# Kernel optimization log

Measured on AMD Instinct MI355X. Metric: run time of the kernel, lower is better.

Reference implementation:

```python
import jax, jax.numpy as jnp
import numpy as np

S, B, D, H = 2048, 2, 1024, 16
DK = D // H
E, F = 8, 4096


def layernorm(x, g, b, eps=1e-5):
    mu = x.mean(-1, keepdims=True)
    var = x.var(-1, keepdims=True)
    return (x - mu) / jnp.sqrt(var + eps) * g + b


def setup_inputs() -> dict:
    key = jax.random.key(0)
    ks = jax.random.split(key, 10)
    s = 0.02
    rn = lambda k, shape: jax.random.normal(k, shape, jnp.float32) * s
    return dict(
        x=jax.random.normal(ks[0], (S, B, D), jnp.float32),
        ln1_g=jnp.ones((D,), jnp.float32), ln1_b=jnp.zeros((D,), jnp.float32),
        ln2_g=jnp.ones((D,), jnp.float32), ln2_b=jnp.zeros((D,), jnp.float32),
        wq=rn(ks[1], (D, D)), bq=jnp.zeros((D,), jnp.float32),
        wk=rn(ks[2], (D, D)), bk=jnp.zeros((D,), jnp.float32),
        wv=rn(ks[3], (D, D)), bv=jnp.zeros((D,), jnp.float32),
        wo=rn(ks[4], (D, D)), bo=jnp.zeros((D,), jnp.float32),
        w_gate=rn(ks[5], (D, E)), b_gate=jnp.zeros((E,), jnp.float32),
        w1=rn(ks[6], (E, D, F)), b1=jnp.zeros((E, F), jnp.float32),
        w2=rn(ks[7], (E, F, D)), b2=jnp.zeros((E, D), jnp.float32),
        mask=jnp.ones((S, S, B), jnp.bool_),
    )


def reference(x, ln1_g, ln1_b, ln2_g, ln2_b, wq, bq, wk, bk, wv, bv, wo, bo,
              w_gate, b_gate, w1, b1, w2, b2, mask):
    scale = 1.0 / np.sqrt(DK).astype(np.float32)
    # --- self attention (pre-norm) ---
    z = layernorm(x, ln1_g, ln1_b)
    q = (z @ wq + bq).reshape(S, B, H, DK)
    k = (z @ wk + bk).reshape(S, B, H, DK)
    v = (z @ wv + bv).reshape(S, B, H, DK)
    scores = jnp.einsum('sbhd,tbhd->stbh', q, k) * scale  # [Sq,Sk,B,H]
    scores = jnp.where(mask[:, :, :, None], scores, -jnp.inf)
    attn = jax.nn.softmax(scores, axis=1)  # softmax over key axis (dim=1)
    o = jnp.einsum('stbh,tbhd->sbhd', attn, v).reshape(S, B, D)
    x = x + (o @ wo + bo)
    # --- switch (top-1) MoE FFN (pre-norm) ---
    z = layernorm(x, ln2_g, ln2_b)
    flat = z.reshape(-1, D)  # [T, D], T = S*B
    probs = jax.nn.softmax(flat @ w_gate + b_gate, axis=-1)  # [T, E]
    pmax = probs.max(-1)
    routes = probs.argmax(-1)
    onehot = jax.nn.one_hot(routes, E, dtype=flat.dtype)  # [T, E]
    # dense dispatch: compute every expert, combine with one-hot mask
    h = jax.nn.relu(jnp.einsum('td,edf->etf', flat, w1) + b1[:, None, :])
    y = jnp.einsum('etf,efd->etd', h, w2) + b2[:, None, :]
    ff = jnp.einsum('etd,te->td', y, onehot) * pmax[:, None]
    out = x + ff.reshape(S, B, D)
    counts = onehot.sum(0)  # tokens per expert
    route_prob_sum = probs.sum(0)
    n_dropped = jnp.array(0, jnp.int32)  # drop_tokens=False
    return out, counts, route_prob_sum, n_dropped, pmax
```

## Files before the change

kernel.cpp:

```cpp
#include <hip/hip_runtime.h>

#define S_LEN 2048
#define B_SZ 2
#define D_DIM 1024
#define H_HEADS 16
#define DK_DIM 64
#define E_EXP 8
#define F_DIM 4096
#define T_TOK 4096

typedef unsigned short ush;
typedef __bf16 bf16x8 __attribute__((ext_vector_type(8)));
typedef float f32x4 __attribute__((ext_vector_type(4)));

__device__ __forceinline__ ush f2bf(float f) {
  union { __bf16 h; ush u; } cv;
  cv.h = (__bf16)f;
  return cv.u;
}

__device__ __forceinline__ float bf2f(ush u) {
  union { unsigned int i; float f; } cv;
  cv.i = ((unsigned int)u) << 16;
  return cv.f;
}

__device__ __forceinline__ void split2(float v, ush& h, ush& l) {
  ush hh = f2bf(v);
  h = hh;
  l = f2bf(v - bf2f(hh));
}

__device__ __forceinline__ void gload16(const void* g, void* l) {
  __builtin_amdgcn_global_load_lds(
      (const __attribute__((address_space(1))) unsigned int*)g,
      (__attribute__((address_space(3))) unsigned int*)l, 16, 0, 0);
}

#define MFMA(a, b, c) __builtin_amdgcn_mfma_f32_16x16x32_bf16(a, b, c, 0, 0, 0)

__global__ __launch_bounds__(256) void ln1_split(const float* __restrict__ x,
    const float* __restrict__ g, const float* __restrict__ b,
    ush* __restrict__ zh, ush* __restrict__ zl) {
  int t = blockIdx.x;
  float4 v = ((const float4*)(x + (size_t)t * D_DIM))[threadIdx.x];
  float s = v.x + v.y + v.z + v.w;
  float s2 = v.x * v.x + v.y * v.y + v.z * v.z + v.w * v.w;
#pragma unroll
  for (int off = 32; off > 0; off >>= 1) {
    s += __shfl_down(s, off);
    s2 += __shfl_down(s2, off);
  }
  __shared__ float red[8];
  int wid = threadIdx.x >> 6;
  if ((threadIdx.x & 63) == 0) { red[wid] = s; red[4 + wid] = s2; }
  __syncthreads();
  float sum = red[0] + red[1] + red[2] + red[3];
  float sq = red[4] + red[5] + red[6] + red[7];
  float mu = sum * (1.0f / D_DIM);
  float var = sq * (1.0f / D_DIM) - mu * mu;
  float rstd = rsqrtf(var + 1e-5f);
  float4 gg = ((const float4*)g)[threadIdx.x];
  float4 bb = ((const float4*)b)[threadIdx.x];
  float o[4];
  o[0] = (v.x - mu) * rstd * gg.x + bb.x;
  o[1] = (v.y - mu) * rstd * gg.y + bb.y;
  o[2] = (v.z - mu) * rstd * gg.z + bb.z;
  o[3] = (v.w - mu) * rstd * gg.w + bb.w;
  ushort4 uh, ul;
  split2(o[0], uh.x, ul.x); split2(o[1], uh.y, ul.y);
  split2(o[2], uh.z, ul.z); split2(o[3], uh.w, ul.w);
  *(ushort4*)(zh + (size_t)t * D_DIM + threadIdx.x * 4) = uh;
  *(ushort4*)(zl + (size_t)t * D_DIM + threadIdx.x * 4) = ul;
}

__global__ __launch_bounds__(256) void transpose_split(const float* __restrict__ in,
    ush* __restrict__ outh, ush* __restrict__ outl, int R, int C) {
  __shared__ float tile[32][33];
  int c0 = blockIdx.x * 32, r0 = blockIdx.y * 32;
  int tx = threadIdx.x & 31, ty = threadIdx.x >> 5;
#pragma unroll
  for (int i = 0; i < 4; i++)
    tile[ty + i * 8][tx] = in[(size_t)(r0 + ty + i * 8) * C + c0 + tx];
  __syncthreads();
#pragma unroll
  for (int i = 0; i < 4; i++) {
    float v = tile[tx][ty + i * 8];
    ush h, l;
    split2(v, h, l);
    size_t idx = (size_t)(c0 + ty + i * 8) * R + r0 + tx;
    outh[idx] = h;
    outl[idx] = l;
  }
}

__global__ __launch_bounds__(256) void transpose_bf16(const float* __restrict__ in,
    ush* __restrict__ out, int R, int C) {
  __shared__ float tile[32][33];
  int e = blockIdx.z;
  const float* ip = in + (size_t)e * R * C;
  ush* op = out + (size_t)e * R * C;
  int c0 = blockIdx.x * 32, r0 = blockIdx.y * 32;
  int tx = threadIdx.x & 31, ty = threadIdx.x >> 5;
#pragma unroll
  for (int i = 0; i < 4; i++)
    tile[ty + i * 8][tx] = ip[(size_t)(r0 + ty + i * 8) * C + c0 + tx];
  __syncthreads();
#pragma unroll
  for (int i = 0; i < 4; i++)
    op[(size_t)(c0 + ty + i * 8) * R + r0 + tx] = f2bf(tile[tx][ty + i * 8]);
}

__device__ __forceinline__ void split_gemm(const ush* __restrict__ Ah,
    const ush* __restrict__ Al, int lda, const ush* __restrict__ Bh,
    const ush* __restrict__ Bl, int ldb, int K, int tid, f32x4 acc[4][4],
    ush (*Ash)[64], ush (*Asl)[64], ush (*Bsh)[64], ush (*Bsl)[64]) {
  int lane = tid & 63, w = tid >> 6, quad = lane >> 4, ln15 = lane & 15;
  int srow = tid >> 3, scol = (tid & 7) * 8;
  int mb = (w >> 1) * 64, nb = (w & 1) * 64;
  for (int kb = 0; kb < K; kb += 64) {
    __syncthreads();
#pragma unroll
    for (int r = 0; r < 4; r++) {
      int rr = r * 32 + srow;
      gload16(Ah + (size_t)rr * lda + kb + scol, &Ash[rr][scol]);
      gload16(Al + (size_t)rr * lda + kb + scol, &Asl[rr][scol]);
      gload16(Bh + (size_t)rr * ldb + kb + scol, &Bsh[rr][scol]);
      gload16(Bl + (size_t)rr * ldb + kb + scol, &Bsl[rr][scol]);
    }
    __syncthreads();
#pragma unroll
    for (int kc = 0; kc < 2; kc++) {
      int kof = kc * 32 + quad * 8;
      bf16x8 avh[4], avl[4], bvh[4], bvl[4];
#pragma unroll
      for (int i = 0; i < 4; i++) {
        avh[i] = *(const bf16x8*)&Ash[mb + i * 16 + ln15][kof];
        avl[i] = *(const bf16x8*)&Asl[mb + i * 16 + ln15][kof];
        bvh[i] = *(const bf16x8*)&Bsh[nb + i * 16 + ln15][kof];
        bvl[i] = *(const bf16x8*)&Bsl[nb + i * 16 + ln15][kof];
      }
#pragma unroll
      for (int mi = 0; mi < 4; mi++)
#pragma unroll
        for (int ni = 0; ni < 4; ni++) {
          acc[mi][ni] = MFMA(avh[mi], bvh[ni], acc[mi][ni]);
          acc[mi][ni] = MFMA(avh[mi], bvl[ni], acc[mi][ni]);
          acc[mi][ni] = MFMA(avl[mi], bvh[ni], acc[mi][ni]);
        }
    }
  }
}

__global__ __launch_bounds__(256) void qkv_mfma(const ush* __restrict__ zh,
    const ush* __restrict__ zl, const ush* __restrict__ wT,
    const float* __restrict__ bq, const float* __restrict__ bk,
    const float* __restrict__ bv, ush* __restrict__ qh_, ush* __restrict__ kh_,
    ush* __restrict__ vth_) {
  __shared__ ush Ash[128][64], Asl[128][64], Bsh[128][64], Bsl[128][64];
  int z = blockIdx.z;
  int m0 = blockIdx.x * 128, n0 = blockIdx.y * 128;
  const ush* Bh = wT + (size_t)z * 2097152;
  const ush* Bl = Bh + 1048576;
  const float* bias = (z == 0) ? bq : (z == 1) ? bk : bv;
  ush* outh = (z == 0) ? qh_ : (z == 1) ? kh_ : vth_;
  int tid = threadIdx.x, lane = tid & 63, w = tid >> 6;
  int quad = lane >> 4, ln15 = lane & 15;
  int mb = (w >> 1) * 64, nb = (w & 1) * 64;
  f32x4 acc[4][4] = {};
  split_gemm(zh + (size_t)m0 * D_DIM, zl + (size_t)m0 * D_DIM, D_DIM,
             Bh + (size_t)n0 * D_DIM, Bl + (size_t)n0 * D_DIM, D_DIM, D_DIM,
             tid, acc, Ash, Asl, Bsh, Bsl);
#pragma unroll
  for (int mi = 0; mi < 4; mi++)
#pragma unroll
    for (int reg = 0; reg < 4; reg++) {
      int m = m0 + mb + mi * 16 + quad * 4 + reg;
      int s = m >> 1, b = m & 1;
#pragma unroll
      for (int ni = 0; ni < 4; ni++) {
        int n = n0 + nb + ni * 16 + ln15;
        float val = acc[mi][ni][reg] + bias[n];
        ush hh, ll;
        split2(val, hh, ll);
        int h = n >> 6, dk = n & 63;
        size_t idx;
        if (z < 2) idx = ((size_t)(b * H_HEADS + h) * S_LEN + s) * DK_DIM + dk;
        else       idx = ((size_t)(b * H_HEADS + h) * DK_DIM + dk) * S_LEN + s;
        outh[idx] = hh;
        outh[idx + 4194304] = ll;
      }
    }
}

__global__ __launch_bounds__(256, 2) void attn_mfma(const ush* __restrict__ qh,
    const ush* __restrict__ ql, const ush* __restrict__ kh,
    const ush* __restrict__ kl, const ush* __restrict__ vth,
    const ush* __restrict__ vtl, ush* __restrict__ oh, ush* __restrict__ ol) {
  int bh = blockIdx.y, q0 = blockIdx.x * 128;
  const size_t hoff = (size_t)bh * S_LEN * DK_DIM;
  __shared__ ush smem[32768];
  ush* Qh_ = smem;
  ush* Ql_ = smem + 8192;
  ush* Kh_ = smem + 16384;
  ush* Kl_ = smem + 20480;
  ush* Vh_ = smem + 24576;
  ush* Vl_ = smem + 28672;
  int tid = threadIdx.x, lane = tid & 63, w = tid >> 6;
  int quad = lane >> 4, ln15 = lane & 15;
  int srow = tid >> 3;
  int schunk = tid & 7;
  int gch = ((schunk ^ (srow & 7))) * 8;
  int sw = ln15 & 7;
#pragma unroll
  for (int p = 0; p < 4; p++) {
    int r = p * 32 + srow;
    gload16(qh + hoff + (size_t)(q0 + r) * DK_DIM + gch, Qh_ + r * 64 + schunk * 8);
    gload16(ql + hoff + (size_t)(q0 + r) * DK_DIM + gch, Ql_ + r * 64 + schunk * 8);
  }
  __syncthreads();
  bf16x8 Qf[2][2][2];
#pragma unroll
  for (int mi = 0; mi < 2; mi++)
#pragma unroll
    for (int kc = 0; kc < 2; kc++) {
      int row = w * 32 + mi * 16 + ln15;
      int ch = ((kc * 4 + quad) ^ sw) * 8;
      Qf[mi][kc][0] = *(const bf16x8*)(Qh_ + row * 64 + ch);
      Qf[mi][kc][1] = *(const bf16x8*)(Ql_ + row * 64 + ch);
    }
  f32x4 Oacc[2][4] = {};
  float m_i[2][4], l_i[2][4];
#pragma unroll
  for (int mi = 0; mi < 2; mi++)
#pragma unroll
    for (int r = 0; r < 4; r++) { m_i[mi][r] = -1e30f; l_i[mi][r] = 0.f; }
  for (int kt = 0; kt < S_LEN / 64; kt++) {
    __syncthreads();
#pragma unroll
    for (int p = 0; p < 2; p++) {
      int r = p * 32 + srow;
      gload16(kh + hoff + (size_t)(kt * 64 + r) * DK_DIM + gch, Kh_ + r * 64 + schunk * 8);
      gload16(kl + hoff + (size_t)(kt * 64 + r) * DK_DIM + gch, Kl_ + r * 64 + schunk * 8);
      gload16(vth + hoff + (size_t)r * S_LEN + kt * 64 + gch, Vh_ + r * 64 + schunk * 8);
      gload16(vtl + hoff + (size_t)r * S_LEN + kt * 64 + gch, Vl_ + r * 64 + schunk * 8);
    }
    __syncthreads();
    f32x4 S[2][4] = {};
#pragma unroll
    for (int kc = 0; kc < 2; kc++) {
      int ch = ((kc * 4 + quad) ^ sw) * 8;
      bf16x8 bkh[4], bkl[4];
#pragma unroll
      for (int ni = 0; ni < 4; ni++) {
        int row = ni * 16 + ln15;
        bkh[ni] = *(const bf16x8*)(Kh_ + row * 64 + ch);
        bkl[ni] = *(const bf16x8*)(Kl_ + row * 64 + ch);
      }
#pragma unroll
      for (int mi = 0; mi < 2; mi++)
#pragma unroll
        for (int ni = 0; ni < 4; ni++) {
          S[mi][ni] = MFMA(Qf[mi][kc][0], bkh[ni], S[mi][ni]);
          S[mi][ni] = MFMA(Qf[mi][kc][0], bkl[ni], S[mi][ni]);
          S[mi][ni] = MFMA(Qf[mi][kc][1], bkh[ni], S[mi][ni]);
        }
    }
#pragma unroll
    for (int mi = 0; mi < 2; mi++)
#pragma unroll
      for (int ni = 0; ni < 4; ni++)
#pragma unroll
        for (int reg = 0; reg < 4; reg++) S[mi][ni][reg] *= 0.125f;
    float mt[2][4];
#pragma unroll
    for (int mi = 0; mi < 2; mi++)
#pragma unroll
      for (int reg = 0; reg < 4; reg++)
        mt[mi][reg] = fmaxf(fmaxf(S[mi][0][reg], S[mi][1][reg]),
                            fmaxf(S[mi][2][reg], S[mi][3][reg]));
#pragma unroll
    for (int x = 1; x < 16; x <<= 1)
#pragma unroll
      for (int mi = 0; mi < 2; mi++)
#pragma unroll
        for (int reg = 0; reg < 4; reg++)
          mt[mi][reg] = fmaxf(mt[mi][reg], __shfl_xor(mt[mi][reg], x));
    float alpha[2][4];
#pragma unroll
    for (int mi = 0; mi < 2; mi++)
#pragma unroll
      for (int reg = 0; reg < 4; reg++) {
        float mnew = fmaxf(m_i[mi][reg], mt[mi][reg]);
        alpha[mi][reg] = expf(m_i[mi][reg] - mnew);
        m_i[mi][reg] = mnew;
      }
    float ls[2][4] = {};
#pragma unroll
    for (int mi = 0; mi < 2; mi++)
#pragma unroll
      for (int ni = 0; ni < 4; ni++)
#pragma unroll
        for (int reg = 0; reg < 4; reg++) {
          float p = expf(S[mi][ni][reg] - m_i[mi][reg]);
          ls[mi][reg] += p;
          ush hh, ll;
          split2(p, hh, ll);
          int row = w * 32 + mi * 16 + quad * 4 + reg;
          int cph = ((ni * 2 + (ln15 >> 3)) ^ ((quad * 4 + reg) & 7)) * 8 + (ln15 & 7);
          Qh_[row * 64 + cph] = hh;
          Ql_[row * 64 + cph] = ll;
        }
#pragma unroll
    for (int x = 1; x < 16; x <<= 1)
#pragma unroll
      for (int mi = 0; mi < 2; mi++)
#pragma unroll
        for (int reg = 0; reg < 4; reg++)
          ls[mi][reg] += __shfl_xor(ls[mi][reg], x);
#pragma unroll
    for (int mi = 0; mi < 2; mi++)
#pragma unroll
      for (int reg = 0; reg < 4; reg++)
        l_i[mi][reg] = l_i[mi][reg] * alpha[mi][reg] + ls[mi][reg];
#pragma unroll
    for (int mi = 0; mi < 2; mi++)
#pragma unroll
      for (int ni = 0; ni < 4; ni++)
#pragma unroll
        for (int reg = 0; reg < 4; reg++) Oacc[mi][ni][reg] *= alpha[mi][reg];
#pragma unroll
    for (int kc = 0; kc < 2; kc++) {
      int ch = ((kc * 4 + quad) ^ sw) * 8;
      bf16x8 aph[2], apl[2], bvh[4], bvl[4];
#pragma unroll
      for (int mi = 0; mi < 2; mi++) {
        int row = w * 32 + mi * 16 + ln15;
        aph[mi] = *(const bf16x8*)(Qh_ + row * 64 + ch);
        apl[mi] = *(const bf16x8*)(Ql_ + row * 64 + ch);
      }
#pragma unroll
      for (int ni = 0; ni < 4; ni++) {
        int row = ni * 16 + ln15;
        bvh[ni] = *(const bf16x8*)(Vh_ + row * 64 + ch);
        bvl[ni] = *(const bf16x8*)(Vl_ + row * 64 + ch);
      }
#pragma unroll
      for (int mi = 0; mi < 2; mi++)
#pragma unroll
        for (int ni = 0; ni < 4; ni++) {
          Oacc[mi][ni] = MFMA(aph[mi], bvh[ni], Oacc[mi][ni]);
          Oacc[mi][ni] = MFMA(aph[mi], bvl[ni], Oacc[mi][ni]);
          Oacc[mi][ni] = MFMA(apl[mi], bvh[ni], Oacc[mi][ni]);
        }
    }
  }
  float inv[2][4];
#pragma unroll
  for (int mi = 0; mi < 2; mi++)
#pragma unroll
    for (int reg = 0; reg < 4; reg++) inv[mi][reg] = 1.0f / l_i[mi][reg];
  int b = bh >> 4, h = bh & 15;
#pragma unroll
  for (int mi = 0; mi < 2; mi++)
#pragma unroll
    for (int ni = 0; ni < 4; ni++)
#pragma unroll
      for (int reg = 0; reg < 4; reg++) {
        float ov = Oacc[mi][ni][reg] * inv[mi][reg];
        int s = q0 + w * 32 + mi * 16 + quad * 4 + reg;
        int col = h * DK_DIM + ni * 16 + ln15;
        size_t idx = (size_t)(s * B_SZ + b) * D_DIM + col;
        ush hh, ll;
        split2(ov, hh, ll);
        oh[idx] = hh;
        ol[idx] = ll;
      }
}

__global__ __launch_bounds__(256) void wo_mfma(const ush* __restrict__ oh,
    const ush* __restrict__ ol, const ush* __restrict__ woTh,
    const float* __restrict__ bo, const float* __restrict__ x,
    float* __restrict__ out) {
  __shared__ ush Ash[128][64], Asl[128][64], Bsh[128][64], Bsl[128][64];
  int m0 = blockIdx.x * 128, n0 = blockIdx.y * 128;
  const ush* Bl = woTh + 1048576;
  int tid = threadIdx.x, lane = tid & 63, w = tid >> 6;
  int quad = lane >> 4, ln15 = lane & 15;
  int mb = (w >> 1) * 64, nb = (w & 1) * 64;
  f32x4 acc[4][4] = {};
  split_gemm(oh + (size_t)m0 * D_DIM, ol + (size_t)m0 * D_DIM, D_DIM,
             woTh + (size_t)n0 * D_DIM, Bl + (size_t)n0 * D_DIM, D_DIM, D_DIM,
             tid, acc, Ash, Asl, Bsh, Bsl);
#pragma unroll
  for (int mi = 0; mi < 4; mi++)
#pragma unroll
    for (int reg = 0; reg < 4; reg++) {
      int m = m0 + mb + mi * 16 + quad * 4 + reg;
#pragma unroll
      for (int ni = 0; ni < 4; ni++) {
        int n = n0 + nb + ni * 16 + ln15;
        size_t idx = (size_t)m * D_DIM + n;
        out[idx] = x[idx] + acc[mi][ni][reg] + bo[n];
      }
    }
}

__global__ __launch_bounds__(256) void moe1_mfma(const ush* __restrict__ zb,
    const ush* __restrict__ w1t, const float* __restrict__ b1,
    const int* __restrict__ list, const int* __restrict__ offs,
    ush* __restrict__ h) {
  int e = blockIdx.x;
  int n0 = blockIdx.y * 128;
  int mhalf = blockIdx.z;
  int off = offs[e], cnt = offs[e + 1] - off;
  __shared__ ush As[128][64], Bs[128][64];
  int tid = threadIdx.x, lane = tid & 63, w = tid >> 6;
  int colb = (lane & 7) * 8;
  int srw = w * 8 + (lane >> 3);
  const ush* gB[4];
  ush* lB[4];
#pragma unroll
  for (int r = 0; r < 4; r++) {
    int row = r * 32 + srw;
    gB[r] = w1t + ((size_t)e * F_DIM + n0 + row) * D_DIM + colb;
    lB[r] = &Bs[row][colb];
  }
  int mb = (w >> 1) * 64, nb = (w & 1) * 64;
  int quad = lane >> 4, ln15 = lane & 15;
  const float* be = b1 + (size_t)e * F_DIM;
  for (int m0 = mhalf * 128; m0 < cnt; m0 += 256) {
    const ush* gA[4];
    ush* lA[4];
#pragma unroll
    for (int r = 0; r < 4; r++) {
      int row = r * 32 + srw;
      int ra = m0 + row; if (ra > cnt - 1) ra = cnt - 1;
      int tok = list[off + ra];
      gA[r] = zb + (size_t)tok * D_DIM + colb;
      lA[r] = &As[row][colb];
    }
    f32x4 acc[4][4] = {};
    for (int kb = 0; kb < D_DIM; kb += 64) {
      __syncthreads();
#pragma unroll
      for (int r = 0; r < 4; r++) { gload16(gA[r] + kb, lA[r]); gload16(gB[r] + kb, lB[r]); }
      __syncthreads();
#pragma unroll
      for (int kc = 0; kc < 2; kc++) {
        int kof = kc * 32 + quad * 8;
        bf16x8 av[4], bv[4];
#pragma unroll
        for (int i = 0; i < 4; i++) {
          av[i] = *(const bf16x8*)&As[mb + i * 16 + ln15][kof];
          bv[i] = *(const bf16x8*)&Bs[nb + i * 16 + ln15][kof];
        }
#pragma unroll
        for (int mi = 0; mi < 4; mi++)
#pragma unroll
          for (int ni = 0; ni < 4; ni++)
            acc[mi][ni] = MFMA(av[mi], bv[ni], acc[mi][ni]);
      }
    }
#pragma unroll
    for (int mi = 0; mi < 4; mi++)
#pragma unroll
      for (int reg = 0; reg < 4; reg++) {
        int lm = m0 + mb + mi * 16 + quad * 4 + reg;
        if (lm < cnt) {
#pragma unroll
          for (int ni = 0; ni < 4; ni++) {
            int n = n0 + nb + ni * 16 + ln15;
            float v = acc[mi][ni][reg] + be[n];
            h[(size_t)(off + lm) * F_DIM + n] = f2bf(fmaxf(v, 0.f));
          }
        }
      }
  }
}

__global__ __launch_bounds__(256) void moe2_mfma(const ush* __restrict__ hb,
    const ush* __restrict__ w2t, const float* __restrict__ b2,
    const int* __restrict__ list, const int* __restrict__ offs,
    const float* __restrict__ pmax, float* __restrict__ out) {
  int e = blockIdx.x;
  int n0 = blockIdx.y * 128;
  int ks = blockIdx.z >> 1;
  int mhalf = blockIdx.z & 1;
  int off = offs[e], cnt = offs[e + 1] - off;
  size_t kbase = (size_t)ks * 1024;
  __shared__ ush As[128][64], Bs[128][64];
  int tid = threadIdx.x, lane = tid & 63, w = tid >> 6;
  int colb = (lane & 7) * 8;
  int srw = w * 8 + (lane >> 3);
  const ush* gB[4];
  ush* lB[4];
#pragma unroll
  for (int r = 0; r < 4; r++) {
    int row = r * 32 + srw;
    gB[r] = w2t + ((size_t)e * D_DIM + n0 + row) * F_DIM + kbase + colb;
    lB[r] = &Bs[row][colb];
  }
  int mb = (w >> 1) * 64, nb = (w & 1) * 64;
  int quad = lane >> 4, ln15 = lane & 15;
  const float* be = b2 + (size_t)e * D_DIM;
  for (int m0 = mhalf * 128; m0 < cnt; m0 += 256) {
    const ush* gA[4];
    ush* lA[4];
#pragma unroll
    for (int r = 0; r < 4; r++) {
      int row = r * 32 + srw;
      int ra = m0 + row; if (ra > cnt - 1) ra = cnt - 1;
      gA[r] = hb + (size_t)(off + ra) * F_DIM + kbase + colb;
      lA[r] = &As[row][colb];
    }
    f32x4 acc[4][4] = {};
    for (int kb = 0; kb < 1024; kb += 64) {
      __syncthreads();
#pragma unroll
      for (int r = 0; r < 4; r++) { gload16(gA[r] + kb, lA[r]); gload16(gB[r] + kb, lB[r]); }
      __syncthreads();
#pragma unroll
      for (int kc = 0; kc < 2; kc++) {
        int kof = kc * 32 + quad * 8;
        bf16x8 av[4], bv[4];
#pragma unroll
        for (int i = 0; i < 4; i++) {
          av[i] = *(const bf16x8*)&As[mb + i * 16 + ln15][kof];
          bv[i] = *(const bf16x8*)&Bs[nb + i * 16 + ln15][kof];
        }
#pragma unroll
        for (int mi = 0; mi < 4; mi++)
#pragma unroll
          for (int ni = 0; ni < 4; ni++)
            acc[mi][ni] = MFMA(av[mi], bv[ni], acc[mi][ni]);
      }
    }
#pragma unroll
    for (int mi = 0; mi < 4; mi++)
#pragma unroll
      for (int reg = 0; reg < 4; reg++) {
        int lm = m0 + mb + mi * 16 + quad * 4 + reg;
        if (lm < cnt) {
          int tok = list[off + lm];
          float p = pmax[tok];
#pragma unroll
          for (int ni = 0; ni < 4; ni++) {
            int n = n0 + nb + ni * 16 + ln15;
            float v = acc[mi][ni][reg];
            if (ks == 0) v += be[n];
            atomicAdd(&out[(size_t)tok * D_DIM + n], v * p);
          }
        }
      }
  }
}

__global__ __launch_bounds__(256) void ln2_gate(const float* __restrict__ x,
    const float* __restrict__ g, const float* __restrict__ b,
    const float* __restrict__ wg, const float* __restrict__ bg,
    ush* __restrict__ zb, float* __restrict__ pmax_out, int* __restrict__ route,
    float* __restrict__ rps_partial) {
  int t = blockIdx.x;
  float4 v = ((const float4*)(x + (size_t)t * D_DIM))[threadIdx.x];
  float s = v.x + v.y + v.z + v.w;
  float s2 = v.x * v.x + v.y * v.y + v.z * v.z + v.w * v.w;
#pragma unroll
  for (int off = 32; off > 0; off >>= 1) {
    s += __shfl_down(s, off);
    s2 += __shfl_down(s2, off);
  }
  __shared__ float red[8];
  int wid = threadIdx.x >> 6;
  if ((threadIdx.x & 63) == 0) { red[wid] = s; red[4 + wid] = s2; }
  __syncthreads();
  float sum = red[0] + red[1] + red[2] + red[3];
  float sq = red[4] + red[5] + red[6] + red[7];
  float mu = sum * (1.0f / D_DIM);
  float var = sq * (1.0f / D_DIM) - mu * mu;
  float rstd = rsqrtf(var + 1e-5f);
  float4 gg = ((const float4*)g)[threadIdx.x];
  float4 bb = ((const float4*)b)[threadIdx.x];
  float zz[4];
  zz[0] = (v.x - mu) * rstd * gg.x + bb.x;
  zz[1] = (v.y - mu) * rstd * gg.y + bb.y;
  zz[2] = (v.z - mu) * rstd * gg.z + bb.z;
  zz[3] = (v.w - mu) * rstd * gg.w + bb.w;
  ushort4 u;
  u.x = f2bf(zz[0]); u.y = f2bf(zz[1]); u.z = f2bf(zz[2]); u.w = f2bf(zz[3]);
  *(ushort4*)(zb + (size_t)t * D_DIM + threadIdx.x * 4) = u;
  int d0 = threadIdx.x * 4;
  float acc[8] = {};
  const float* w0 = wg + (size_t)d0 * E_EXP;
#pragma unroll
  for (int i = 0; i < 4; i++)
#pragma unroll
    for (int e = 0; e < 8; e++)
      acc[e] += zz[i] * w0[i * 8 + e];
#pragma unroll
  for (int off = 32; off > 0; off >>= 1)
#pragma unroll
    for (int e = 0; e < 8; e++) acc[e] += __shfl_down(acc[e], off);
  __shared__ float red2[4][8];
  if ((threadIdx.x & 63) == 0)
#pragma unroll
    for (int e = 0; e < 8; e++) red2[threadIdx.x >> 6][e] = acc[e];
  __syncthreads();
  if (threadIdx.x == 0) {
    float lg[8];
#pragma unroll
    for (int e = 0; e < 8; e++)
      lg[e] = red2[0][e] + red2[1][e] + red2[2][e] + red2[3][e] + bg[e];
    float mx = lg[0];
    int am = 0;
#pragma unroll
    for (int e = 1; e < 8; e++)
      if (lg[e] > mx) { mx = lg[e]; am = e; }
    float se = 0.f, pe[8];
#pragma unroll
    for (int e = 0; e < 8; e++) { pe[e] = expf(lg[e] - mx); se += pe[e]; }
    float inv = 1.0f / se;
    pmax_out[t] = inv;
    route[t] = am;
#pragma unroll
    for (int e = 0; e < 8; e++) rps_partial[(size_t)t * 8 + e] = pe[e] * inv;
  }
}

__global__ __launch_bounds__(256) void reduce_gate(const float* __restrict__ rps_partial,
    const int* __restrict__ route, float* __restrict__ rps, int* __restrict__ counts) {
  int e = blockIdx.x;
  float s = 0.f;
  int c = 0;
  for (int t = threadIdx.x; t < T_TOK; t += 256) {
    s += rps_partial[(size_t)t * 8 + e];
    c += (route[t] == e) ? 1 : 0;
  }
#pragma unroll
  for (int off = 32; off > 0; off >>= 1) {
    s += __shfl_down(s, off);
    c += __shfl_down(c, off);
  }
  __shared__ float sred[4];
  __shared__ int cred[4];
  int wid = threadIdx.x >> 6;
  if ((threadIdx.x & 63) == 0) { sred[wid] = s; cred[wid] = c; }
  __syncthreads();
  if (threadIdx.x == 0) {
    rps[e] = sred[0] + sred[1] + sred[2] + sred[3];
    counts[e] = cred[0] + cred[1] + cred[2] + cred[3];
  }
}

__global__ void init_kernel(int* cursor) {
  int i = threadIdx.x;
  if (i < E_EXP) cursor[i] = 0;
}

__global__ void offsets_kernel(const int* counts, int* offs, float* counts_f, float* ndrop) {
  if (threadIdx.x == 0) {
    int o = 0;
    for (int e = 0; e < E_EXP; e++) { offs[e] = o; o += counts[e]; }
    offs[E_EXP] = o;
    for (int e = 0; e < E_EXP; e++) counts_f[e] = (float)counts[e];
    *ndrop = 0.f;
  }
}

__global__ void scatter_kernel(const int* __restrict__ route, const int* __restrict__ offs,
                               int* __restrict__ cursor, int* __restrict__ list) {
  int t = blockIdx.x * 256 + threadIdx.x;
  int lane = threadIdx.x & 63;
  int e = (t < T_TOK) ? route[t] : -1;
#pragma unroll
  for (int ex = 0; ex < E_EXP; ex++) {
    unsigned long long mask = __ballot(e == ex);
    int cntw = __popcll(mask);
    if (cntw) {
      int leader = __ffsll((unsigned long long)mask) - 1;
      int base = 0;
      if (lane == leader) base = atomicAdd(&cursor[ex], cntw);
      base = __shfl(base, leader);
      if (e == ex) {
        int rank = __popcll(mask & ((1ull << lane) - 1));
        list[offs[ex] + base + rank] = t;
      }
    }
  }
}

extern "C" void kernel_launch(void* const* d_in, const int* in_sizes, int n_in,
                              void* d_out, int out_size, void* d_ws, size_t ws_size,
                              hipStream_t stream) {
  const float* x = (const float*)d_in[0];
  const float* ln1_g = (const float*)d_in[1];
  const float* ln1_b = (const float*)d_in[2];
  const float* ln2_g = (const float*)d_in[3];
  const float* ln2_b = (const float*)d_in[4];
  const float* wq = (const float*)d_in[5];
  const float* bq = (const float*)d_in[6];
  const float* wk = (const float*)d_in[7];
  const float* bk = (const float*)d_in[8];
  const float* wv = (const float*)d_in[9];
  const float* bv = (const float*)d_in[10];
  const float* wo = (const float*)d_in[11];
  const float* bo = (const float*)d_in[12];
  const float* wg = (const float*)d_in[13];
  const float* bg = (const float*)d_in[14];
  const float* w1 = (const float*)d_in[15];
  const float* b1 = (const float*)d_in[16];
  const float* w2 = (const float*)d_in[17];
  const float* b2 = (const float*)d_in[18];

  float* out = (float*)d_out;
  float* counts_f = out + (size_t)T_TOK * D_DIM;
  float* rps = counts_f + E_EXP;
  float* ndrop = rps + E_EXP;
  float* pmax = ndrop + 1;

  const size_t MB1 = 1048576;
  char* base = (char*)d_ws;
  ush* zh  = (ush*)(base + 0 * MB1);
  ush* zl  = (ush*)(base + 8 * MB1);
  ush* qh  = (ush*)(base + 16 * MB1);
  ush* ql  = (ush*)(base + 24 * MB1);
  ush* kh  = (ush*)(base + 32 * MB1);
  ush* kl  = (ush*)(base + 40 * MB1);
  ush* vth = (ush*)(base + 48 * MB1);
  ush* vtl = (ush*)(base + 56 * MB1);
  ush* wT  = (ush*)(base + 64 * MB1);
  ush* oh  = (ush*)(base + 80 * MB1);
  ush* ol  = (ush*)(base + 88 * MB1);
  ush* zb  = (ush*)(base + 64 * MB1);
  ush* hb  = (ush*)(base + 72 * MB1);
  int* route  = (int*)(base + 104 * MB1);
  int* list   = route + T_TOK;
  int* counts = list + T_TOK;
  int* offs   = counts + E_EXP;
  int* cursor = offs + E_EXP + 1;
  float* rps_partial = (float*)(base + 106 * MB1);
  ush* w1t = (ush*)(base + 0 * MB1);
  ush* w2t = (ush*)(base + 112 * MB1);

  ln1_split<<<T_TOK, 256, 0, stream>>>(x, ln1_g, ln1_b, zh, zl);
  dim3 gt(32, 32);
  transpose_split<<<gt, 256, 0, stream>>>(wq, wT + 0 * 2097152, wT + 0 * 2097152 + 1048576, D_DIM, D_DIM);
  transpose_split<<<gt, 256, 0, stream>>>(wk, wT + 1 * 2097152, wT + 1 * 2097152 + 1048576, D_DIM, D_DIM);
  transpose_split<<<gt, 256, 0, stream>>>(wv, wT + 2 * 2097152, wT + 2 * 2097152 + 1048576, D_DIM, D_DIM);
  transpose_split<<<gt, 256, 0, stream>>>(wo, wT + 3 * 2097152, wT + 3 * 2097152 + 1048576, D_DIM, D_DIM);
  dim3 gq(32, 8, 3);
  qkv_mfma<<<gq, 256, 0, stream>>>(zh, zl, wT, bq, bk, bv, qh, kh, vth);
  dim3 ga(S_LEN / 128, B_SZ * H_HEADS);
  attn_mfma<<<ga, 256, 0, stream>>>(qh, ql, kh, kl, vth, vtl, oh, ol);
  dim3 gt1(F_DIM / 32, D_DIM / 32, E_EXP);
  transpose_bf16<<<gt1, 256, 0, stream>>>(w1, w1t, D_DIM, F_DIM);
  dim3 gt2(D_DIM / 32, F_DIM / 32, E_EXP);
  transpose_bf16<<<gt2, 256, 0, stream>>>(w2, w2t, F_DIM, D_DIM);
  dim3 gw(32, 8);
  wo_mfma<<<gw, 256, 0, stream>>>(oh, ol, wT + 3 * 2097152, bo, x, out);
  init_kernel<<<1, 64, 0, stream>>>(cursor);
  ln2_gate<<<T_TOK, 256, 0, stream>>>(out, ln2_g, ln2_b, wg, bg, zb, pmax, route, rps_partial);
  reduce_gate<<<E_EXP, 256, 0, stream>>>(rps_partial, route, rps, counts);
  offsets_kernel<<<1, 64, 0, stream>>>(counts, offs, counts_f, ndrop);
  scatter_kernel<<<16, 256, 0, stream>>>(route, offs, cursor, list);
  dim3 gm1(E_EXP, F_DIM / 128, 2);
  moe1_mfma<<<gm1, 256, 0, stream>>>(zb, w1t, b1, list, offs, hb);
  dim3 gm2(E_EXP, D_DIM / 128, 8);
  moe2_mfma<<<gm2, 256, 0, stream>>>(hb, w2t, b2, list, offs, pmax, out);
}
```

Before: 977.3 us.

## Prefetch K/V tiles into registers and use lazy softmax rescaling in attention

Replaces the synchronous global-to-shared K/V loads with a register prefetch of the next tile, overlapping global memory latency with the current tile's compute. The softmax now folds the 1/sqrt(dk) scale into an exp2 argument and rescales O and l only when some row max grows past a threshold. It also moves the row-sum shuffle reduction after the PV MFMAs and raises wave priority around MFMA blocks. The tradeoffs are higher register pressure from the prefetch buffers and possible larger intermediate exponents before a rescale.

```diff
diff --git a/kernel.cpp b/kernel.cpp
--- a/kernel.cpp
+++ b/kernel.cpp
@@ -199,7 +199,7 @@
     const ush* __restrict__ vtl, ush* __restrict__ oh, ush* __restrict__ ol) {
   int bh = blockIdx.y, q0 = blockIdx.x * 128;
   const size_t hoff = (size_t)bh * S_LEN * DK_DIM;
-  __shared__ ush smem[32768];
+  __shared__ __align__(16) ush smem[32768];
   ush* Qh_ = smem;
   ush* Ql_ = smem + 8192;
   ush* Kh_ = smem + 16384;
@@ -229,23 +229,42 @@
       Qf[mi][kc][0] = *(const bf16x8*)(Qh_ + row * 64 + ch);
       Qf[mi][kc][1] = *(const bf16x8*)(Ql_ + row * 64 + ch);
     }
+  const ush* pkh = kh + hoff + (size_t)srow * DK_DIM + schunk * 8;
+  const ush* pkl = kl + hoff + (size_t)srow * DK_DIM + schunk * 8;
+  const ush* pvh = vth + hoff + (size_t)srow * S_LEN + schunk * 8;
+  const ush* pvl = vtl + hoff + (size_t)srow * S_LEN + schunk * 8;
+  int ldst = srow * 64 + gch;
+  float4 pk[2][2], pv[2][2];
+#define LOAD_KV(KT) do {                                                       \
+    size_t ko = (size_t)(KT) * (64 * DK_DIM);                                  \
+    size_t vo = (size_t)(KT) * 64;                                             \
+    _Pragma("unroll")                                                          \
+    for (int p = 0; p < 2; p++) {                                              \
+      pk[p][0] = *(const float4*)(pkh + ko + p * 32 * DK_DIM);                 \
+      pk[p][1] = *(const float4*)(pkl + ko + p * 32 * DK_DIM);                 \
+      pv[p][0] = *(const float4*)(pvh + vo + (size_t)p * 32 * S_LEN);          \
+      pv[p][1] = *(const float4*)(pvl + vo + (size_t)p * 32 * S_LEN);          \
+    }                                                                          \
+  } while (0)
+  LOAD_KV(0);
   f32x4 Oacc[2][4] = {};
   float m_i[2][4], l_i[2][4];
 #pragma unroll
   for (int mi = 0; mi < 2; mi++)
 #pragma unroll
-    for (int r = 0; r < 4; r++) { m_i[mi][r] = -1e30f; l_i[mi][r] = 0.f; }
+    for (int r = 0; r < 4; r++) { m_i[mi][r] = -3e38f; l_i[mi][r] = 0.f; }
+  const float cs = 0.18033688f;
   for (int kt = 0; kt < S_LEN / 64; kt++) {
     __syncthreads();
 #pragma unroll
     for (int p = 0; p < 2; p++) {
-      int r = p * 32 + srow;
-      gload16(kh + hoff + (size_t)(kt * 64 + r) * DK_DIM + gch, Kh_ + r * 64 + schunk * 8);
-      gload16(kl + hoff + (size_t)(kt * 64 + r) * DK_DIM + gch, Kl_ + r * 64 + schunk * 8);
-      gload16(vth + hoff + (size_t)r * S_LEN + kt * 64 + gch, Vh_ + r * 64 + schunk * 8);
-      gload16(vtl + hoff + (size_t)r * S_LEN + kt * 64 + gch, Vl_ + r * 64 + schunk * 8);
+      *(float4*)(Kh_ + p * 2048 + ldst) = pk[p][0];
+      *(float4*)(Kl_ + p * 2048 + ldst) = pk[p][1];
+      *(float4*)(Vh_ + p * 2048 + ldst) = pv[p][0];
+      *(float4*)(Vl_ + p * 2048 + ldst) = pv[p][1];
     }
     __syncthreads();
+    if (kt + 1 < S_LEN / 64) LOAD_KV(kt + 1);
     f32x4 S[2][4] = {};
 #pragma unroll
     for (int kc = 0; kc < 2; kc++) {
@@ -257,6 +276,7 @@
         bkh[ni] = *(const bf16x8*)(Kh_ + row * 64 + ch);
         bkl[ni] = *(const bf16x8*)(Kl_ + row * 64 + ch);
       }
+      __builtin_amdgcn_s_setprio(1);
 #pragma unroll
       for (int mi = 0; mi < 2; mi++)
 #pragma unroll
@@ -265,13 +285,8 @@
           S[mi][ni] = MFMA(Qf[mi][kc][0], bkl[ni], S[mi][ni]);
           S[mi][ni] = MFMA(Qf[mi][kc][1], bkh[ni], S[mi][ni]);
         }
-    }
-#pragma unroll
-    for (int mi = 0; mi < 2; mi++)
-#pragma unroll
-      for (int ni = 0; ni < 4; ni++)
-#pragma unroll
-        for (int reg = 0; reg < 4; reg++) S[mi][ni][reg] *= 0.125f;
+      __builtin_amdgcn_s_setprio(0);
+    }
     float mt[2][4];
 #pragma unroll
     for (int mi = 0; mi < 2; mi++)
@@ -286,23 +301,38 @@
 #pragma unroll
         for (int reg = 0; reg < 4; reg++)
           mt[mi][reg] = fmaxf(mt[mi][reg], __shfl_xor(mt[mi][reg], x));
-    float alpha[2][4];
+    float growth = -3e38f;
 #pragma unroll
     for (int mi = 0; mi < 2; mi++)
 #pragma unroll
-      for (int reg = 0; reg < 4; reg++) {
-        float mnew = fmaxf(m_i[mi][reg], mt[mi][reg]);
-        alpha[mi][reg] = expf(m_i[mi][reg] - mnew);
-        m_i[mi][reg] = mnew;
-      }
-    float ls[2][4] = {};
+      for (int reg = 0; reg < 4; reg++)
+        growth = fmaxf(growth, mt[mi][reg] - m_i[mi][reg]);
+    if (__any(growth > 44.3614195f)) {
+#pragma unroll
+      for (int mi = 0; mi < 2; mi++)
+#pragma unroll
+        for (int reg = 0; reg < 4; reg++) {
+          float mnew = fmaxf(m_i[mi][reg], mt[mi][reg]);
+          float a = __builtin_amdgcn_exp2f(cs * (m_i[mi][reg] - mnew));
+          m_i[mi][reg] = mnew;
+          l_i[mi][reg] *= a;
+#pragma unroll
+          for (int ni = 0; ni < 4; ni++) Oacc[mi][ni][reg] *= a;
+        }
+    }
+    float ncm[2][4], ls[2][4] = {};
 #pragma unroll
     for (int mi = 0; mi < 2; mi++)
 #pragma unroll
+      for (int reg = 0; reg < 4; reg++) ncm[mi][reg] = cs * m_i[mi][reg];
+#pragma unroll
+    for (int mi = 0; mi < 2; mi++)
+#pragma unroll
       for (int ni = 0; ni < 4; ni++)
 #pragma unroll
         for (int reg = 0; reg < 4; reg++) {
-          float p = expf(S[mi][ni][reg] - m_i[mi][reg]);
+          float p = __builtin_amdgcn_exp2f(
+              fmaf(S[mi][ni][reg], cs, -ncm[mi][reg]));
           ls[mi][reg] += p;
           ush hh, ll;
           split2(p, hh, ll);
@@ -312,24 +342,6 @@
           Ql_[row * 64 + cph] = ll;
         }
 #pragma unroll
-    for (int x = 1; x < 16; x <<= 1)
-#pragma unroll
-      for (int mi = 0; mi < 2; mi++)
-#pragma unroll
-        for (int reg = 0; reg < 4; reg++)
-          ls[mi][reg] += __shfl_xor(ls[mi][reg], x);
-#pragma unroll
-    for (int mi = 0; mi < 2; mi++)
-#pragma unroll
-      for (int reg = 0; reg < 4; reg++)
-        l_i[mi][reg] = l_i[mi][reg] * alpha[mi][reg] + ls[mi][reg];
-#pragma unroll
-    for (int mi = 0; mi < 2; mi++)
-#pragma unroll
-      for (int ni = 0; ni < 4; ni++)
-#pragma unroll
-        for (int reg = 0; reg < 4; reg++) Oacc[mi][ni][reg] *= alpha[mi][reg];
-#pragma unroll
     for (int kc = 0; kc < 2; kc++) {
       int ch = ((kc * 4 + quad) ^ sw) * 8;
       bf16x8 aph[2], apl[2], bvh[4], bvl[4];
@@ -345,6 +357,7 @@
         bvh[ni] = *(const bf16x8*)(Vh_ + row * 64 + ch);
         bvl[ni] = *(const bf16x8*)(Vl_ + row * 64 + ch);
       }
+      __builtin_amdgcn_s_setprio(1);
 #pragma unroll
       for (int mi = 0; mi < 2; mi++)
 #pragma unroll
@@ -353,8 +366,22 @@
           Oacc[mi][ni] = MFMA(aph[mi], bvl[ni], Oacc[mi][ni]);
           Oacc[mi][ni] = MFMA(apl[mi], bvh[ni], Oacc[mi][ni]);
         }
-    }
-  }
+      __builtin_amdgcn_s_setprio(0);
+    }
+#pragma unroll
+    for (int x = 1; x < 16; x <<= 1)
+#pragma unroll
+      for (int mi = 0; mi < 2; mi++)
+#pragma unroll
+        for (int reg = 0; reg < 4; reg++)
+          ls[mi][reg] += __shfl_xor(ls[mi][reg], x);
+#pragma unroll
+    for (int mi = 0; mi < 2; mi++)
+#pragma unroll
+      for (int reg = 0; reg < 4; reg++)
+        l_i[mi][reg] += ls[mi][reg];
+  }
+#undef LOAD_KV
   float inv[2][4];
 #pragma unroll
   for (int mi = 0; mi < 2; mi++)
```

After: 984.4 us. No clear change (+0.7%).
